# Optimization experiments

Hardware: AMD Instinct MI355X
Metric: run time of the kernel (lower is better)

Reference implementation:

```python
import jax, jax.numpy as jnp
import numpy as np

N = 50000
E = 1000000
WIDTH = 64
DEPTH = 4


def setup_inputs() -> dict:
    key = jax.random.key(0)
    ks = jax.random.split(key, 6)
    x = jax.random.normal(ks[0], (N, 5), dtype=jnp.float32)
    edge_index = jax.random.randint(ks[1], (2, E), 0, N, dtype=jnp.int32)
    edge_attr = jax.random.normal(ks[2], (E, 3), dtype=jnp.float32)
    w1 = jax.random.normal(ks[3], (3, WIDTH), dtype=jnp.float32) / jnp.sqrt(3.0)
    b1 = jnp.zeros((WIDTH,), jnp.float32)
    w2 = jax.random.normal(ks[4], (WIDTH, 1), dtype=jnp.float32) / jnp.sqrt(float(WIDTH))
    b2 = jnp.zeros((1,), jnp.float32)
    root = jax.random.normal(ks[5], (1, 1), dtype=jnp.float32)
    bias = jnp.zeros((1,), jnp.float32)
    return dict(x=x, edge_index=edge_index, edge_attr=edge_attr,
                w1=w1, b1=b1, w2=w2, b2=b2, root=root, bias=bias)


def reference(x, edge_index, edge_attr, w1, b1, w2, b2, root, bias):
    # h: scalar node feature, column 2 of data.x -> [N, 1]
    h = x[:, 2:3]
    src, dst = edge_index[0], edge_index[1]  # messages flow src -> dst

    # Per-edge 1x1 weight from the edge MLP (depends only on edge_attr,
    # identical for all depth iterations since the conv is shared).
    w_e = jax.nn.relu(edge_attr @ w1 + b1) @ w2 + b2  # [E, 1]

    # Mean aggregation: precompute in-degree of each target node.
    deg = jax.ops.segment_sum(jnp.ones((E,), jnp.float32), dst, num_segments=N)
    inv_deg = jnp.where(deg > 0, 1.0 / jnp.maximum(deg, 1.0), 0.0)[:, None]  # [N, 1]

    for _ in range(DEPTH):
        msg = h[src] * w_e                                        # gather + per-edge weight, [E, 1]
        agg = jax.ops.segment_sum(msg, dst, num_segments=N) * inv_deg  # scatter-mean, [N, 1]
        h = jax.nn.relu(agg + h @ root + bias)                    # root transform + bias + ReLU
    return h
```

## Files before the change

### kernel.cpp

```cpp
#include <hip/hip_runtime.h>

#define NN 50000
#define NE 1000000
#define NBK 196
#define ESTRIDE 5632
#define EPB3 5120

#define EPB 1024
#define PB 977

__global__ __launch_bounds__(1024)
void place3(const float* __restrict__ x,
            const float* __restrict__ ea,
            const int* __restrict__ src,
            const int* __restrict__ dst,
            const float* __restrict__ w1,
            const float* __restrict__ b1,
            const float* __restrict__ w2,
            const float* __restrict__ b2,
            uint2* __restrict__ es,
            int* __restrict__ cursor,
            float* __restrict__ hA) {
    __shared__ float sw1[192];
    __shared__ float sb1[64];
    __shared__ float sw2[64];
    __shared__ int hist[NBK];
    __shared__ int hbase[NBK];
    const int t = threadIdx.x;
    const int j = blockIdx.x;
    if (t < 192) sw1[t] = w1[t];
    if (t < 64) { sb1[t] = b1[t]; sw2[t] = w2[t]; }
    if (t < NBK) hist[t] = 0;
    {
        int i = j * 1024 + t;
        if (i < NN) hA[i] = x[5 * i + 2];
    }
    __syncthreads();
    const float bz = b2[0];

    float ce[5];
    int dd[5], rr[5], ss[5];
#pragma unroll
    for (int k = 0; k < 5; ++k) {
        int e = j * EPB3 + k * 1024 + t;
        dd[k] = -1;
        if (e < NE) {
            float a0 = ea[3 * e + 0];
            float a1 = ea[3 * e + 1];
            float a2 = ea[3 * e + 2];
            float c0 = bz, c1 = 0.f, c2 = 0.f, c3 = 0.f;
#pragma unroll
            for (int kk = 0; kk < 64; kk += 4) {
                float h0 = fmaf(a0, sw1[kk+0], fmaf(a1, sw1[64+kk+0], fmaf(a2, sw1[128+kk+0], sb1[kk+0])));
                float h1 = fmaf(a0, sw1[kk+1], fmaf(a1, sw1[64+kk+1], fmaf(a2, sw1[128+kk+1], sb1[kk+1])));
                float h2 = fmaf(a0, sw1[kk+2], fmaf(a1, sw1[64+kk+2], fmaf(a2, sw1[128+kk+2], sb1[kk+2])));
                float h3 = fmaf(a0, sw1[kk+3], fmaf(a1, sw1[64+kk+3], fmaf(a2, sw1[128+kk+3], sb1[kk+3])));
                c0 = fmaf(fmaxf(h0, 0.f), sw2[kk+0], c0);
                c1 = fmaf(fmaxf(h1, 0.f), sw2[kk+1], c1);
                c2 = fmaf(fmaxf(h2, 0.f), sw2[kk+2], c2);
                c3 = fmaf(fmaxf(h3, 0.f), sw2[kk+3], c3);
            }
            ce[k] = (c0 + c1) + (c2 + c3);
            ss[k] = src[e];
            int d = dst[e];
            dd[k] = d;
            rr[k] = atomicAdd(&hist[d >> 8], 1);
        }
    }
    __syncthreads();
    if (t < NBK) {
        int hv = hist[t];
        hbase[t] = hv ? atomicAdd(&cursor[t], hv) : 0;
    }
    __syncthreads();
#pragma unroll
    for (int k = 0; k < 5; ++k) {
        if (dd[k] >= 0) {
            int d = dd[k];
            int b = d >> 8;
            int prel = hbase[b] + rr[k];
            int pos = (prel < ESTRIDE) ? (b * ESTRIDE + prel)
                                       : (NBK * ESTRIDE + (t & 63));
            es[pos] = make_uint2((unsigned)ss[k] | ((unsigned)(d & 255) << 17),
                                 __float_as_uint(ce[k]));
        }
    }
}

template<int FIRST>
__global__ __launch_bounds__(1024)
void round_fused(const int* __restrict__ curRel,
                 const uint2* __restrict__ es,
                 const float* __restrict__ hold,
                 float* __restrict__ hnew,
                 float* __restrict__ invdeg,
                 const float* __restrict__ root,
                 const float* __restrict__ bias) {
    __shared__ float lagg[256];
    __shared__ int ldeg[256];
    int t = threadIdx.x;
    int b = blockIdx.x;
    if (t < 256) { lagg[t] = 0.f; if (FIRST) ldeg[t] = 0; }
    __syncthreads();
    int s0 = b * ESTRIDE;
    int cnt = curRel[b];
    if (cnt > ESTRIDE) cnt = ESTRIDE;
    int s1 = s0 + cnt;
    const uint4* es4 = (const uint4*)es;
    for (int p = s0 + t * 2; p < s1; p += 2048) {
        uint4 v = es4[p >> 1];
        {
            int sidx = v.x & 0x1FFFF;
            int dl = (v.x >> 17) & 255;
            atomicAdd(&lagg[dl], hold[sidx] * __uint_as_float(v.y));
            if (FIRST) atomicAdd(&ldeg[dl], 1);
        }
        if (p + 1 < s1) {
            int sidx = v.z & 0x1FFFF;
            int dl = (v.z >> 17) & 255;
            atomicAdd(&lagg[dl], hold[sidx] * __uint_as_float(v.w));
            if (FIRST) atomicAdd(&ldeg[dl], 1);
        }
    }
    __syncthreads();
    if (t < 256) {
        int node = b * 256 + t;
        if (node < NN) {
            float inv;
            if (FIRST) {
                int d = ldeg[t];
                inv = (d > 0) ? (1.0f / (float)d) : 0.f;
                invdeg[node] = inv;
            } else {
                inv = invdeg[node];
            }
            hnew[node] = fmaxf(fmaf(hold[node], root[0], fmaf(lagg[t], inv, bias[0])), 0.f);
        }
    }
}

__global__ void bucket_count(const int* __restrict__ dst, int* __restrict__ bcnt,
                             const float* __restrict__ x, float* __restrict__ h) {
    __shared__ int hist[NBK];
    int t = threadIdx.x;
    if (t < NBK) hist[t] = 0;
    __syncthreads();
    int gid = blockIdx.x * 256 + t;
    if (gid < NN) h[gid] = x[5 * gid + 2];
#pragma unroll
    for (int j = 0; j < 4; ++j) {
        int e = blockIdx.x * EPB + j * 256 + t;
        if (e < NE) atomicAdd(&hist[dst[e] >> 8], 1);
    }
    __syncthreads();
    if (t < NBK && hist[t]) atomicAdd(&bcnt[t], hist[t]);
}

__global__ void bucket_scan(const int* __restrict__ bcnt,
                            int* __restrict__ sBeg,
                            int* __restrict__ cursor,
                            int* __restrict__ sLim) {
    __shared__ int part[256];
    int t = threadIdx.x;
    int v = (t < NBK) ? ((bcnt[t] + 1) & ~1) : 0;
    part[t] = v;
    __syncthreads();
    for (int off = 1; off < 256; off <<= 1) {
        int x = part[t];
        int add = (t >= off) ? part[t - off] : 0;
        __syncthreads();
        part[t] = x + add;
        __syncthreads();
    }
    if (t < NBK) {
        int excl = part[t] - v;
        sBeg[t] = excl;
        cursor[t] = excl;
        sLim[t] = 0x7FFFFFFF;
    }
}

__global__ void place_kernel(const float* __restrict__ ea,
                             const int* __restrict__ src,
                             const int* __restrict__ dst,
                             const float* __restrict__ w1,
                             const float* __restrict__ b1,
                             const float* __restrict__ w2,
                             const float* __restrict__ b2,
                             const int* __restrict__ sLim,
                             int* __restrict__ cursor,
                             uint2* __restrict__ es,
                             int dumpbase) {
    __shared__ float sw1[192];
    __shared__ float sb1[64];
    __shared__ float sw2[64];
    __shared__ float sce[EPB];
    __shared__ int hist[NBK];
    __shared__ int hbase[NBK];
    int t = threadIdx.x;
    if (t < 192) sw1[t] = w1[t];
    if (t < 64) { sb1[t] = b1[t]; sw2[t] = w2[t]; }
    if (t < NBK) hist[t] = 0;
    __syncthreads();

    int r[4], dd[4];
#pragma unroll
    for (int j = 0; j < 4; ++j) {
        int e = blockIdx.x * EPB + j * 256 + t;
        dd[j] = -1;
        if (e < NE) {
            float a0 = ea[3 * e + 0];
            float a1 = ea[3 * e + 1];
            float a2 = ea[3 * e + 2];
            float c0 = b2[0], c1 = 0.f, c2 = 0.f, c3 = 0.f;
#pragma unroll
            for (int k = 0; k < 64; k += 4) {
                float h0 = fmaf(a0, sw1[k+0], fmaf(a1, sw1[64+k+0], fmaf(a2, sw1[128+k+0], sb1[k+0])));
                float h1 = fmaf(a0, sw1[k+1], fmaf(a1, sw1[64+k+1], fmaf(a2, sw1[128+k+1], sb1[k+1])));
                float h2 = fmaf(a0, sw1[k+2], fmaf(a1, sw1[64+k+2], fmaf(a2, sw1[128+k+2], sb1[k+2])));
                float h3 = fmaf(a0, sw1[k+3], fmaf(a1, sw1[64+k+3], fmaf(a2, sw1[128+k+3], sb1[k+3])));
                c0 = fmaf(fmaxf(h0, 0.f), sw2[k+0], c0);
                c1 = fmaf(fmaxf(h1, 0.f), sw2[k+1], c1);
                c2 = fmaf(fmaxf(h2, 0.f), sw2[k+2], c2);
                c3 = fmaf(fmaxf(h3, 0.f), sw2[k+3], c3);
            }
            sce[j * 256 + t] = (c0 + c1) + (c2 + c3);
            int d = dst[e];
            dd[j] = d;
            r[j] = atomicAdd(&hist[d >> 8], 1);
        }
    }
    __syncthreads();
    if (t < NBK) { int hv = hist[t]; if (hv) hbase[t] = atomicAdd(&cursor[t], hv); }
    __syncthreads();
#pragma unroll
    for (int j = 0; j < 4; ++j) {
        int e = blockIdx.x * EPB + j * 256 + t;
        if (e < NE) {
            int d = dd[j];
            int b = d >> 8;
            int pos = hbase[b] + r[j];
            if (pos >= sLim[b]) pos = dumpbase + (t & 63);
            unsigned pack = (unsigned)src[e] | ((unsigned)(d & 255) << 17);
            es[pos] = make_uint2(pack, __float_as_uint(sce[j * 256 + t]));
        }
    }
}

template<int FIRST>
__global__ __launch_bounds__(1024)
void round_fused_fb(const int* __restrict__ sBeg,
                    const int* __restrict__ sEnd,
                    const int* __restrict__ sLim,
                    const uint2* __restrict__ es,
                    const float* __restrict__ hold,
                    float* __restrict__ hnew,
                    float* __restrict__ invdeg,
                    const float* __restrict__ root,
                    const float* __restrict__ bias) {
    __shared__ float lagg[256];
    __shared__ int ldeg[256];
    int t = threadIdx.x;
    int b = blockIdx.x;
    if (t < 256) { lagg[t] = 0.f; if (FIRST) ldeg[t] = 0; }
    __syncthreads();
    int s0 = sBeg[b];
    int s1 = sEnd[b];
    { int cap = sLim[b]; if (s1 > cap) s1 = cap; }
    const uint4* es4 = (const uint4*)es;
    for (int p = s0 + t * 2; p < s1; p += 2048) {
        uint4 v = es4[p >> 1];
        {
            int sidx = v.x & 0x1FFFF;
            int dl = (v.x >> 17) & 255;
            atomicAdd(&lagg[dl], hold[sidx] * __uint_as_float(v.y));
            if (FIRST) atomicAdd(&ldeg[dl], 1);
        }
        if (p + 1 < s1) {
            int sidx = v.z & 0x1FFFF;
            int dl = (v.z >> 17) & 255;
            atomicAdd(&lagg[dl], hold[sidx] * __uint_as_float(v.w));
            if (FIRST) atomicAdd(&ldeg[dl], 1);
        }
    }
    __syncthreads();
    if (t < 256) {
        int node = b * 256 + t;
        if (node < NN) {
            float inv;
            if (FIRST) {
                int d = ldeg[t];
                inv = (d > 0) ? (1.0f / (float)d) : 0.f;
                invdeg[node] = inv;
            } else {
                inv = invdeg[node];
            }
            hnew[node] = fmaxf(fmaf(hold[node], root[0], fmaf(lagg[t], inv, bias[0])), 0.f);
        }
    }
}


extern "C" void kernel_launch(void* const* d_in, const int* in_sizes, int n_in,
                              void* d_out, int out_size, void* d_ws, size_t ws_size,
                              hipStream_t stream) {
    const float* x    = (const float*)d_in[0];
    const int*   ei   = (const int*)d_in[1];
    const float* ea   = (const float*)d_in[2];
    const float* w1   = (const float*)d_in[3];
    const float* b1   = (const float*)d_in[4];
    const float* w2   = (const float*)d_in[5];
    const float* b2   = (const float*)d_in[6];
    const float* root = (const float*)d_in[7];
    const float* bias = (const float*)d_in[8];

    const int* src = ei;
    const int* dst = ei + NE;
    float* out = (float*)d_out;

    const size_t esN = (size_t)NBK * ESTRIDE + 64;
    const size_t needFixed = esN * 8
                           + (size_t)NBK * 4
                           + (size_t)NN * 4 * 3;

    if (ws_size >= needFixed) {
        uint2* es     = (uint2*)d_ws;
        int*   cursor = (int*)(es + esN);
        float* invdeg = (float*)(cursor + NBK);
        float* hA     = invdeg + NN;
        float* hB     = hA + NN;

        hipMemsetAsync(cursor, 0, NBK * 4, stream);
        place3<<<NBK, 1024, 0, stream>>>(x, ea, src, dst, w1, b1, w2, b2,
                                         es, cursor, hA);
        round_fused<1><<<NBK, 1024, 0, stream>>>(cursor, es, hA, hB, invdeg, root, bias);
        round_fused<0><<<NBK, 1024, 0, stream>>>(cursor, es, hB, hA, invdeg, root, bias);
        round_fused<0><<<NBK, 1024, 0, stream>>>(cursor, es, hA, hB, invdeg, root, bias);
        round_fused<0><<<NBK, 1024, 0, stream>>>(cursor, es, hB, out, invdeg, root, bias);
    } else {
        uint2* es     = (uint2*)d_ws;
        int*   bcnt   = (int*)(es + NE + NBK);
        int*   cursor = bcnt + NBK;
        int*   sBeg   = cursor + NBK;
        int*   sLim   = sBeg + NBK;
        float* invdeg = (float*)(sLim + NBK);
        float* hB     = invdeg + NN;
        float* h      = out;

        hipMemsetAsync(bcnt, 0, NBK * 4, stream);
        bucket_count<<<PB, 256, 0, stream>>>(dst, bcnt, x, h);
        bucket_scan<<<1, 256, 0, stream>>>(bcnt, sBeg, cursor, sLim);
        place_kernel<<<PB, 256, 0, stream>>>(ea, src, dst, w1, b1, w2, b2,
                                             sLim, cursor, es, 0);
        round_fused_fb<1><<<NBK, 1024, 0, stream>>>(sBeg, cursor, sLim, es, h,  hB, invdeg, root, bias);
        round_fused_fb<0><<<NBK, 1024, 0, stream>>>(sBeg, cursor, sLim, es, hB, h,  invdeg, root, bias);
        round_fused_fb<0><<<NBK, 1024, 0, stream>>>(sBeg, cursor, sLim, es, h,  hB, invdeg, root, bias);
        round_fused_fb<0><<<NBK, 1024, 0, stream>>>(sBeg, cursor, sLim, es, hB, h,  invdeg, root, bias);
    }
}
```

Baseline: 144.5 us.

## Sort bucketed edges into per-node CSR and aggregate with 8-lane segmented reduction

```diff
diff --git a/kernel.cpp b/kernel.cpp
--- a/kernel.cpp
+++ b/kernel.cpp
@@ -1,6 +1,7 @@
 #include <hip/hip_runtime.h>
 
 #define NN 50000
+#define NNP 50176
 #define NE 1000000
 #define NBK 196
 #define ESTRIDE 5632
@@ -87,55 +88,83 @@
     }
 }
 
-template<int FIRST>
 __global__ __launch_bounds__(1024)
-void round_fused(const int* __restrict__ curRel,
+void reorder_csr(const int* __restrict__ cursor,
                  const uint2* __restrict__ es,
-                 const float* __restrict__ hold,
-                 float* __restrict__ hnew,
-                 float* __restrict__ invdeg,
-                 const float* __restrict__ root,
-                 const float* __restrict__ bias) {
-    __shared__ float lagg[256];
-    __shared__ int ldeg[256];
-    int t = threadIdx.x;
-    int b = blockIdx.x;
-    if (t < 256) { lagg[t] = 0.f; if (FIRST) ldeg[t] = 0; }
-    __syncthreads();
-    int s0 = b * ESTRIDE;
-    int cnt = curRel[b];
+                 uint2* __restrict__ es2,
+                 uint2* __restrict__ nodePtr) {
+    __shared__ int hist[256];
+    __shared__ int part[256];
+    __shared__ int cur[256];
+    const int t = threadIdx.x;
+    const int b = blockIdx.x;
+    if (t < 256) hist[t] = 0;
+    __syncthreads();
+    const int s0 = b * ESTRIDE;
+    int cnt = cursor[b];
     if (cnt > ESTRIDE) cnt = ESTRIDE;
-    int s1 = s0 + cnt;
-    const uint4* es4 = (const uint4*)es;
-    for (int p = s0 + t * 2; p < s1; p += 2048) {
-        uint4 v = es4[p >> 1];
-        {
-            int sidx = v.x & 0x1FFFF;
-            int dl = (v.x >> 17) & 255;
-            atomicAdd(&lagg[dl], hold[sidx] * __uint_as_float(v.y));
-            if (FIRST) atomicAdd(&ldeg[dl], 1);
-        }
-        if (p + 1 < s1) {
-            int sidx = v.z & 0x1FFFF;
-            int dl = (v.z >> 17) & 255;
-            atomicAdd(&lagg[dl], hold[sidx] * __uint_as_float(v.w));
-            if (FIRST) atomicAdd(&ldeg[dl], 1);
-        }
-    }
-    __syncthreads();
+
+    uint2 v[6]; int key[6]; bool m[6];
+#pragma unroll
+    for (int k = 0; k < 6; ++k) {
+        int p = k * 1024 + t;
+        m[k] = (p < cnt);
+        if (m[k]) {
+            v[k] = es[s0 + p];
+            key[k] = (v[k].x >> 17) & 255;
+            atomicAdd(&hist[key[k]], 1);
+        }
+    }
+    __syncthreads();
+    int val = 0;
+    if (t < 256) { val = hist[t]; part[t] = val; }
+    __syncthreads();
+    for (int off = 1; off < 256; off <<= 1) {
+        int xv = 0, add = 0;
+        if (t < 256) { xv = part[t]; if (t >= off) add = part[t - off]; }
+        __syncthreads();
+        if (t < 256) part[t] = xv + add;
+        __syncthreads();
+    }
     if (t < 256) {
-        int node = b * 256 + t;
-        if (node < NN) {
-            float inv;
-            if (FIRST) {
-                int d = ldeg[t];
-                inv = (d > 0) ? (1.0f / (float)d) : 0.f;
-                invdeg[node] = inv;
-            } else {
-                inv = invdeg[node];
-            }
-            hnew[node] = fmaxf(fmaf(hold[node], root[0], fmaf(lagg[t], inv, bias[0])), 0.f);
-        }
+        int excl = part[t] - val;
+        cur[t] = excl;
+        nodePtr[b * 256 + t] = make_uint2((unsigned)(s0 + excl), (unsigned)val);
+    }
+    __syncthreads();
+#pragma unroll
+    for (int k = 0; k < 6; ++k) {
+        if (m[k]) {
+            int pos = atomicAdd(&cur[key[k]], 1);
+            es2[s0 + pos] = v[k];
+        }
+    }
+}
+
+__global__ __launch_bounds__(256)
+void round_csr(const uint2* __restrict__ nodePtr,
+               const uint2* __restrict__ es2,
+               const float* __restrict__ hold,
+               float* __restrict__ hnew,
+               const float* __restrict__ root,
+               const float* __restrict__ bias) {
+    int g = blockIdx.x * 256 + threadIdx.x;
+    int row = g >> 3;
+    int sub = g & 7;
+    uint2 pk = nodePtr[row];
+    int beg = (int)pk.x;
+    int len = (int)pk.y;
+    float acc = 0.f;
+    for (int k = sub; k < len; k += 8) {
+        uint2 v = es2[beg + k];
+        acc += hold[v.x & 0x1FFFF] * __uint_as_float(v.y);
+    }
+    acc += __shfl_xor(acc, 1);
+    acc += __shfl_xor(acc, 2);
+    acc += __shfl_xor(acc, 4);
+    if (sub == 0 && row < NN) {
+        float inv = (len > 0) ? (1.0f / (float)len) : 0.f;
+        hnew[row] = fmaxf(fmaf(hold[row], root[0], fmaf(acc, inv, bias[0])), 0.f);
     }
 }
 
@@ -320,23 +349,28 @@
 
     const size_t esN = (size_t)NBK * ESTRIDE + 64;
     const size_t needFixed = esN * 8
+                           + (size_t)NBK * ESTRIDE * 8
+                           + (size_t)NNP * 8
                            + (size_t)NBK * 4
-                           + (size_t)NN * 4 * 3;
+                           + (size_t)NN * 4 * 2;
 
     if (ws_size >= needFixed) {
-        uint2* es     = (uint2*)d_ws;
-        int*   cursor = (int*)(es + esN);
-        float* invdeg = (float*)(cursor + NBK);
-        float* hA     = invdeg + NN;
-        float* hB     = hA + NN;
+        uint2* es      = (uint2*)d_ws;
+        uint2* es2     = es + esN;
+        uint2* nodePtr = es2 + (size_t)NBK * ESTRIDE;
+        int*   cursor  = (int*)(nodePtr + NNP);
+        float* hA      = (float*)(cursor + NBK);
+        float* hB      = hA + NN;
 
         hipMemsetAsync(cursor, 0, NBK * 4, stream);
         place3<<<NBK, 1024, 0, stream>>>(x, ea, src, dst, w1, b1, w2, b2,
                                          es, cursor, hA);
-        round_fused<1><<<NBK, 1024, 0, stream>>>(cursor, es, hA, hB, invdeg, root, bias);
-        round_fused<0><<<NBK, 1024, 0, stream>>>(cursor, es, hB, hA, invdeg, root, bias);
-        round_fused<0><<<NBK, 1024, 0, stream>>>(cursor, es, hA, hB, invdeg, root, bias);
-        round_fused<0><<<NBK, 1024, 0, stream>>>(cursor, es, hB, out, invdeg, root, bias);
+        reorder_csr<<<NBK, 1024, 0, stream>>>(cursor, es, es2, nodePtr);
+        const int gR = NNP * 8 / 256;
+        round_csr<<<gR, 256, 0, stream>>>(nodePtr, es2, hA, hB, root, bias);
+        round_csr<<<gR, 256, 0, stream>>>(nodePtr, es2, hB, hA, root, bias);
+        round_csr<<<gR, 256, 0, stream>>>(nodePtr, es2, hA, hB, root, bias);
+        round_csr<<<gR, 256, 0, stream>>>(nodePtr, es2, hB, out, root, bias);
     } else {
         uint2* es     = (uint2*)d_ws;
         int*   bcnt   = (int*)(es + NE + NBK);
```

After: 143.6 us. About the same (-0.6%).
